# Kernel optimization log

Measured on AMD Instinct MI355X. Metric: run time of the kernel, lower is better.

## Reference

```python
import jax, jax.numpy as jnp
import numpy as np

B, H, S, D = 4, 16, 2048, 128
HIDDEN_DIM = 128  # init arg; used as softmax scale


def setup_inputs() -> dict:
    key = jax.random.key(0)
    kq, kk, kv = jax.random.split(key, 3)
    q = jax.random.normal(kq, (B, H, S, D), dtype=jnp.float32)
    k = jax.random.normal(kk, (B, H, S, D), dtype=jnp.float32)
    v = jax.random.normal(kv, (B, H, S, D), dtype=jnp.float32)
    return {"q": q, "k": k, "v": v}


def reference(q, k, v):
    # scores[b,h,s,t] = sum_d q[b,h,s,d] * k[b,h,t,d]  (y permuted on last two dims, then matmul)
    scores = jnp.einsum("bhsd,bhtd->bhst", q, k) * (HIDDEN_DIM ** -0.5)
    probs = jax.nn.softmax(scores, axis=-1)
    return jnp.einsum("bhst,bhtd->bhsd", probs, v)
```

## Files before the change

kernel.cpp:

```cpp
#include <hip/hip_runtime.h>
#include <hip/hip_bf16.h>


#define SEQ 2048
#define DH  128
#define NBH 64
#define BM  64
#define BN  64
#define QK_LD 136
#define VT_LD 72
#define P_LD  72
#define THR 8.0f

typedef __attribute__((ext_vector_type(8))) short short8;
typedef __attribute__((ext_vector_type(4))) float f32x4;

#if __has_builtin(__builtin_amdgcn_exp2f)
#define EXP2F(x) __builtin_amdgcn_exp2f(x)
#else
#define EXP2F(x) exp2f(x)
#endif

#define CS (0.08838834764831845f * 1.44269504088896340736f)

__device__ __forceinline__ unsigned int pk_bf16(float lo, float hi) {
    union { __hip_bfloat162 h; unsigned int u; } cv;
    cv.h = __float22bfloat162_rn(make_float2(lo, hi));
    return cv.u;
}

__global__ __launch_bounds__(256) void transpose_v_kernel(
        const float* __restrict__ v, unsigned short* __restrict__ vt) {
    __shared__ float tile[64][65];
    const int bh = blockIdx.z;
    const int s0 = blockIdx.x * 64;
    const int d0 = blockIdx.y * 64;
    const int tid = threadIdx.x;
    const float* src = v + ((size_t)bh * SEQ + s0) * DH + d0;
#pragma unroll
    for (int i = 0; i < 4; ++i) {
        int id  = tid + 256 * i;
        int row = id >> 4;
        int c4  = (id & 15) << 2;
        float4 val = *reinterpret_cast<const float4*>(src + row * DH + c4);
        tile[row][c4 + 0] = val.x;
        tile[row][c4 + 1] = val.y;
        tile[row][c4 + 2] = val.z;
        tile[row][c4 + 3] = val.w;
    }
    __syncthreads();
    unsigned short* dst = vt + ((size_t)bh * DH + d0) * SEQ + s0;
#pragma unroll
    for (int i = 0; i < 2; ++i) {
        int id = tid + 256 * i;
        int dd = id >> 3;
        int kc = (id & 7) << 3;
        uint4 pk;
        unsigned int* pw = reinterpret_cast<unsigned int*>(&pk);
#pragma unroll
        for (int j = 0; j < 4; ++j)
            pw[j] = pk_bf16(tile[kc + 2 * j][dd], tile[kc + 2 * j + 1][dd]);
        *reinterpret_cast<uint4*>(dst + (size_t)dd * SEQ + kc) = pk;
    }
}

__global__ __launch_bounds__(256) void convert_k_kernel(
        const float* __restrict__ k, unsigned short* __restrict__ kb) {
    size_t base = ((size_t)blockIdx.x * 256 + threadIdx.x) * 8;
    float4 a = *reinterpret_cast<const float4*>(k + base);
    float4 b = *reinterpret_cast<const float4*>(k + base + 4);
    uint4 o;
    o.x = pk_bf16(a.x, a.y);
    o.y = pk_bf16(a.z, a.w);
    o.z = pk_bf16(b.x, b.y);
    o.w = pk_bf16(b.z, b.w);
    *reinterpret_cast<uint4*>(kb + base) = o;
}

template<bool KPRE>
__global__ __launch_bounds__(256, 3) void fattn_kernel(
        const float* __restrict__ q, const float* __restrict__ kf,
        const unsigned short* __restrict__ kb,
        const unsigned short* __restrict__ vt, float* __restrict__ out) {
    __shared__ unsigned short Ks[BN * QK_LD];
    __shared__ unsigned short Vs[DH * VT_LD];
    __shared__ unsigned short Ps[BM * P_LD];

    const int wid = ((blockIdx.x & 7) << 8) | (blockIdx.x >> 3);
    const int bh  = wid >> 5;
    const int q0  = (wid & 31) * BM;
    const int tid  = threadIdx.x;
    const int w    = tid >> 6;
    const int lane = tid & 63;
    const int l15  = lane & 15;
    const int quad = lane >> 4;

    short8 qf[4];
    {
        const float* qptr = q + ((size_t)bh * SEQ + q0 + w * 16 + l15) * DH + quad * 8;
#pragma unroll
        for (int kk = 0; kk < 4; ++kk) {
            float4 x = *reinterpret_cast<const float4*>(qptr + kk * 32);
            float4 y = *reinterpret_cast<const float4*>(qptr + kk * 32 + 4);
            union { short8 s; uint4 u; } cv;
            cv.u.x = pk_bf16(x.x * CS, x.y * CS);
            cv.u.y = pk_bf16(x.z * CS, x.w * CS);
            cv.u.z = pk_bf16(y.x * CS, y.y * CS);
            cv.u.w = pk_bf16(y.z * CS, y.w * CS);
            qf[kk] = cv.s;
        }
    }

    f32x4 o[8];
#pragma unroll
    for (int t = 0; t < 8; ++t) o[t] = (f32x4){0.f, 0.f, 0.f, 0.f};
    float mrow[4] = {-1e30f, -1e30f, -1e30f, -1e30f};
    float lrow[4] = {0.f, 0.f, 0.f, 0.f};

    const float*          kfp = kf + (size_t)bh * SEQ * DH;
    const unsigned short* kbp = kb + (size_t)bh * SEQ * DH;
    const unsigned short* vptr = vt + (size_t)bh * DH * SEQ;

    unsigned int* Ps32 = reinterpret_cast<unsigned int*>(Ps);
    const int prow_base = w * 16 + quad * 4;
    const int pdw = (l15 & 1) ? (8 + (l15 >> 1)) : (l15 >> 1);

    for (int kt = 0; kt < SEQ / BN; ++kt) {
        const int k0 = kt * BN;
        if (KPRE) {
#pragma unroll
            for (int i = 0; i < 4; ++i) {
                int id  = tid + 256 * i;
                int row = id >> 4;
                int c   = (id & 15) << 3;
                *reinterpret_cast<uint4*>(&Ks[row * QK_LD + c]) =
                    *reinterpret_cast<const uint4*>(kbp + (size_t)(k0 + row) * DH + c);
            }
        } else {
#pragma unroll
            for (int i = 0; i < 8; ++i) {
                int id  = tid + 256 * i;
                int row = id >> 5;
                int c4  = (id & 31) << 2;
                float4 val = *reinterpret_cast<const float4*>(kfp + (size_t)(k0 + row) * DH + c4);
                uint2 pk;
                pk.x = pk_bf16(val.x, val.y);
                pk.y = pk_bf16(val.z, val.w);
                *reinterpret_cast<uint2*>(&Ks[row * QK_LD + c4]) = pk;
            }
        }
#pragma unroll
        for (int i = 0; i < 4; ++i) {
            int id = tid + 256 * i;
            int dd = id >> 3;
            int kc = (id & 7) << 3;
            *reinterpret_cast<uint4*>(&Vs[dd * VT_LD + kc]) =
                *reinterpret_cast<const uint4*>(vptr + (size_t)dd * SEQ + k0 + kc);
        }
        __syncthreads();

        f32x4 acc[4];
#pragma unroll
        for (int t = 0; t < 4; ++t) acc[t] = (f32x4){0.f, 0.f, 0.f, 0.f};
#pragma unroll
        for (int kk = 0; kk < 4; ++kk) {
            const int koff = kk * 32 + quad * 8;
#pragma unroll
            for (int t = 0; t < 4; ++t) {
                short8 b = *reinterpret_cast<const short8*>(&Ks[(t * 16 + l15) * QK_LD + koff]);
                acc[t] = __builtin_amdgcn_mfma_f32_16x16x32_bf16(qf[kk], b, acc[t], 0, 0, 0);
            }
        }

        float lm[4];
#pragma unroll
        for (int r = 0; r < 4; ++r)
            lm[r] = fmaxf(fmaxf(acc[0][r], acc[1][r]), fmaxf(acc[2][r], acc[3][r]));
        float need = fmaxf(fmaxf(lm[0] - mrow[0], lm[1] - mrow[1]),
                           fmaxf(lm[2] - mrow[2], lm[3] - mrow[3]));
        if (__any(need > THR)) {
#pragma unroll
            for (int r = 0; r < 4; ++r) {
                float mx = lm[r];
#pragma unroll
                for (int off = 1; off < 16; off <<= 1)
                    mx = fmaxf(mx, __shfl_xor(mx, off));
                float mnew  = fmaxf(mrow[r], mx);
                float alpha = EXP2F(mrow[r] - mnew);
                mrow[r] = mnew;
                lrow[r] *= alpha;
#pragma unroll
                for (int t = 0; t < 8; ++t) o[t][r] *= alpha;
            }
        }

#pragma unroll
        for (int r = 0; r < 4; ++r) {
            float p0 = EXP2F(acc[0][r] - mrow[r]);
            float p1 = EXP2F(acc[1][r] - mrow[r]);
            float p2 = EXP2F(acc[2][r] - mrow[r]);
            float p3 = EXP2F(acc[3][r] - mrow[r]);
            lrow[r] += (p0 + p1) + (p2 + p3);
            unsigned int a01 = pk_bf16(p0, p1);
            unsigned int a23 = pk_bf16(p2, p3);
            unsigned int s01 = __shfl_xor((int)a01, 1);
            unsigned int s23 = __shfl_xor((int)a23, 1);
            unsigned int w0, w1;
            if (l15 & 1) {
                w0 = (s01 >> 16) | (a01 & 0xffff0000u);
                w1 = (s23 >> 16) | (a23 & 0xffff0000u);
            } else {
                w0 = (a01 & 0xffffu) | (s01 << 16);
                w1 = (a23 & 0xffffu) | (s23 << 16);
            }
            const int dw = (prow_base + r) * (P_LD / 2) + pdw;
            Ps32[dw]      = w0;
            Ps32[dw + 16] = w1;
        }

#pragma unroll
        for (int kk = 0; kk < 2; ++kk) {
            const int koff = kk * 32 + quad * 8;
            short8 a = *reinterpret_cast<const short8*>(&Ps[(w * 16 + l15) * P_LD + koff]);
#pragma unroll
            for (int t = 0; t < 8; ++t) {
                short8 b = *reinterpret_cast<const short8*>(&Vs[(t * 16 + l15) * VT_LD + koff]);
                o[t] = __builtin_amdgcn_mfma_f32_16x16x32_bf16(a, b, o[t], 0, 0, 0);
            }
        }
        __syncthreads();
    }

#pragma unroll
    for (int r = 0; r < 4; ++r) {
#pragma unroll
        for (int off = 1; off < 16; off <<= 1)
            lrow[r] += __shfl_xor(lrow[r], off);
    }
    float* obase = out + ((size_t)bh * SEQ + q0) * DH;
#pragma unroll
    for (int r = 0; r < 4; ++r) {
        float inv = 1.0f / lrow[r];
        int row = w * 16 + quad * 4 + r;
#pragma unroll
        for (int t = 0; t < 8; ++t)
            obase[(size_t)row * DH + t * 16 + l15] = o[t][r] * inv;
    }
}

extern "C" void kernel_launch(void* const* d_in, const int* in_sizes, int n_in,
                              void* d_out, int out_size, void* d_ws, size_t ws_size,
                              hipStream_t stream) {
    const float* q = (const float*)d_in[0];
    const float* k = (const float*)d_in[1];
    const float* v = (const float*)d_in[2];
    float* out = (float*)d_out;
    unsigned short* vt = (unsigned short*)d_ws;

    transpose_v_kernel<<<dim3(SEQ / 64, DH / 64, NBH), dim3(256), 0, stream>>>(v, vt);

    const size_t vt_elems = (size_t)NBH * SEQ * DH;
    if (ws_size >= 2 * vt_elems * sizeof(unsigned short)) {
        unsigned short* kbuf = vt + vt_elems;
        convert_k_kernel<<<dim3((NBH * SEQ * DH) / (256 * 8)), dim3(256), 0, stream>>>(k, kbuf);
        fattn_kernel<true><<<dim3(SEQ / BM * NBH), dim3(256), 0, stream>>>(q, nullptr, kbuf, vt, out);
    } else {
        fattn_kernel<false><<<dim3(SEQ / BM * NBH), dim3(256), 0, stream>>>(q, k, nullptr, vt, out);
    }
}
```

Measured before the change: 435.7 us.

## Fuse K conversion into V transpose kernel and register-prefetch next K/V tile

Merges the K fp32-to-bf16 conversion into the V transpose prep kernel, which removes one kernel launch. In the attention loop, the next K and V tiles are now loaded into registers while the current tile is being computed, then written to LDS after the compute finishes. The aim is to hide global load latency behind the MFMA work. In exchange it raises register pressure, which may hurt occupancy under launch_bounds(256,3), and adds an extra barrier on every iteration.

```diff
diff --git a/kernel.cpp b/kernel.cpp
--- a/kernel.cpp
+++ b/kernel.cpp
@@ -7,6 +7,7 @@
 #define NBH 64
 #define BM  64
 #define BN  64
+#define NT  (SEQ / BN)
 #define QK_LD 136
 #define VT_LD 72
 #define P_LD  72
@@ -29,13 +30,30 @@
     return cv.u;
 }
 
-__global__ __launch_bounds__(256) void transpose_v_kernel(
-        const float* __restrict__ v, unsigned short* __restrict__ vt) {
+template<bool DOK>
+__global__ __launch_bounds__(256) void prep_kernel(
+        const float* __restrict__ v, unsigned short* __restrict__ vt,
+        const float* __restrict__ k, unsigned short* __restrict__ kb) {
     __shared__ float tile[64][65];
     const int bh = blockIdx.z;
     const int s0 = blockIdx.x * 64;
     const int d0 = blockIdx.y * 64;
     const int tid = threadIdx.x;
+
+    if (DOK) {
+        const size_t kbase = ((size_t)blockIdx.x +
+                              32 * ((size_t)blockIdx.y + 2 * (size_t)blockIdx.z)) * 4096;
+#pragma unroll
+        for (int i = 0; i < 4; ++i) {
+            size_t idx = kbase + ((size_t)tid + 256 * i) * 4;
+            float4 val = *reinterpret_cast<const float4*>(k + idx);
+            uint2 pk;
+            pk.x = pk_bf16(val.x, val.y);
+            pk.y = pk_bf16(val.z, val.w);
+            *reinterpret_cast<uint2*>(kb + idx) = pk;
+        }
+    }
+
     const float* src = v + ((size_t)bh * SEQ + s0) * DH + d0;
 #pragma unroll
     for (int i = 0; i < 4; ++i) {
@@ -64,19 +82,6 @@
     }
 }
 
-__global__ __launch_bounds__(256) void convert_k_kernel(
-        const float* __restrict__ k, unsigned short* __restrict__ kb) {
-    size_t base = ((size_t)blockIdx.x * 256 + threadIdx.x) * 8;
-    float4 a = *reinterpret_cast<const float4*>(k + base);
-    float4 b = *reinterpret_cast<const float4*>(k + base + 4);
-    uint4 o;
-    o.x = pk_bf16(a.x, a.y);
-    o.y = pk_bf16(a.z, a.w);
-    o.z = pk_bf16(b.x, b.y);
-    o.w = pk_bf16(b.z, b.w);
-    *reinterpret_cast<uint4*>(kb + base) = o;
-}
-
 template<bool KPRE>
 __global__ __launch_bounds__(256, 3) void fattn_kernel(
         const float* __restrict__ q, const float* __restrict__ kf,
@@ -117,25 +122,51 @@
     float mrow[4] = {-1e30f, -1e30f, -1e30f, -1e30f};
     float lrow[4] = {0.f, 0.f, 0.f, 0.f};
 
-    const float*          kfp = kf + (size_t)bh * SEQ * DH;
-    const unsigned short* kbp = kb + (size_t)bh * SEQ * DH;
+    const float*          kfp  = kf + (size_t)bh * SEQ * DH;
+    const unsigned short* kbp  = kb + (size_t)bh * SEQ * DH;
     const unsigned short* vptr = vt + (size_t)bh * DH * SEQ;
 
     unsigned int* Ps32 = reinterpret_cast<unsigned int*>(Ps);
     const int prow_base = w * 16 + quad * 4;
     const int pdw = (l15 & 1) ? (8 + (l15 >> 1)) : (l15 >> 1);
 
-    for (int kt = 0; kt < SEQ / BN; ++kt) {
+    uint4 kreg[4], vreg[4];
+    const int krow = tid >> 4, kcol = (tid & 15) << 3;
+    const int vrow = tid >> 3, vcol = (tid & 7) << 3;
+
+#define LOAD_TILE(KT)                                                          \
+    do {                                                                       \
+        const int _k0 = (KT) * BN;                                             \
+        _Pragma("unroll")                                                      \
+        for (int i = 0; i < 4; ++i)                                            \
+            kreg[i] = *reinterpret_cast<const uint4*>(                         \
+                kbp + (size_t)(_k0 + krow + 16 * i) * DH + kcol);              \
+        _Pragma("unroll")                                                      \
+        for (int i = 0; i < 4; ++i)                                            \
+            vreg[i] = *reinterpret_cast<const uint4*>(                         \
+                vptr + (size_t)(vrow + 32 * i) * SEQ + _k0 + vcol);            \
+    } while (0)
+
+#define WRITE_TILE()                                                           \
+    do {                                                                       \
+        _Pragma("unroll")                                                      \
+        for (int i = 0; i < 4; ++i)                                            \
+            *reinterpret_cast<uint4*>(&Ks[(krow + 16 * i) * QK_LD + kcol]) = kreg[i]; \
+        _Pragma("unroll")                                                      \
+        for (int i = 0; i < 4; ++i)                                            \
+            *reinterpret_cast<uint4*>(&Vs[(vrow + 32 * i) * VT_LD + vcol]) = vreg[i]; \
+    } while (0)
+
+    if (KPRE) {
+        LOAD_TILE(0);
+        WRITE_TILE();
+        __syncthreads();
+    }
+
+    for (int kt = 0; kt < NT; ++kt) {
         const int k0 = kt * BN;
         if (KPRE) {
-#pragma unroll
-            for (int i = 0; i < 4; ++i) {
-                int id  = tid + 256 * i;
-                int row = id >> 4;
-                int c   = (id & 15) << 3;
-                *reinterpret_cast<uint4*>(&Ks[row * QK_LD + c]) =
-                    *reinterpret_cast<const uint4*>(kbp + (size_t)(k0 + row) * DH + c);
-            }
+            if (kt + 1 < NT) LOAD_TILE(kt + 1);
         } else {
 #pragma unroll
             for (int i = 0; i < 8; ++i) {
@@ -148,16 +179,16 @@
                 pk.y = pk_bf16(val.z, val.w);
                 *reinterpret_cast<uint2*>(&Ks[row * QK_LD + c4]) = pk;
             }
-        }
-#pragma unroll
-        for (int i = 0; i < 4; ++i) {
-            int id = tid + 256 * i;
-            int dd = id >> 3;
-            int kc = (id & 7) << 3;
-            *reinterpret_cast<uint4*>(&Vs[dd * VT_LD + kc]) =
-                *reinterpret_cast<const uint4*>(vptr + (size_t)dd * SEQ + k0 + kc);
-        }
-        __syncthreads();
+#pragma unroll
+            for (int i = 0; i < 4; ++i) {
+                int id = tid + 256 * i;
+                int dd = id >> 3;
+                int kc = (id & 7) << 3;
+                *reinterpret_cast<uint4*>(&Vs[dd * VT_LD + kc]) =
+                    *reinterpret_cast<const uint4*>(vptr + (size_t)dd * SEQ + k0 + kc);
+            }
+            __syncthreads();
+        }
 
         f32x4 acc[4];
 #pragma unroll
@@ -229,6 +260,10 @@
             }
         }
         __syncthreads();
+        if (KPRE) {
+            if (kt + 1 < NT) WRITE_TILE();
+            __syncthreads();
+        }
     }
 
 #pragma unroll
@@ -257,14 +292,13 @@
     float* out = (float*)d_out;
     unsigned short* vt = (unsigned short*)d_ws;
 
-    transpose_v_kernel<<<dim3(SEQ / 64, DH / 64, NBH), dim3(256), 0, stream>>>(v, vt);
-
     const size_t vt_elems = (size_t)NBH * SEQ * DH;
     if (ws_size >= 2 * vt_elems * sizeof(unsigned short)) {
         unsigned short* kbuf = vt + vt_elems;
-        convert_k_kernel<<<dim3((NBH * SEQ * DH) / (256 * 8)), dim3(256), 0, stream>>>(k, kbuf);
+        prep_kernel<true><<<dim3(SEQ / 64, DH / 64, NBH), dim3(256), 0, stream>>>(v, vt, k, kbuf);
         fattn_kernel<true><<<dim3(SEQ / BM * NBH), dim3(256), 0, stream>>>(q, nullptr, kbuf, vt, out);
     } else {
+        prep_kernel<false><<<dim3(SEQ / 64, DH / 64, NBH), dim3(256), 0, stream>>>(v, vt, nullptr, nullptr);
         fattn_kernel<false><<<dim3(SEQ / BM * NBH), dim3(256), 0, stream>>>(q, k, nullptr, vt, out);
     }
 }
```

Result: slower. 831.3 us (+90.8%).
